# Kernel optimization log

Hardware: AMD Instinct MI355X
Metric: run time of the kernel (lower is better)

## Reference

```python
import jax, jax.numpy as jnp
import numpy as np

D_MODEL = 2048
N_HEADS = 16
D_HEAD = D_MODEL // N_HEADS  # 128
WINDOW = 512
SCALE = D_HEAD ** -0.5


def setup_inputs() -> dict:
    key = jax.random.key(0)
    ks = jax.random.split(key, 5)
    B, S = 2, 4096
    x = jax.random.normal(ks[0], (B, S, D_MODEL), dtype=jnp.float32)
    W_qkv = jax.random.normal(ks[1], (D_MODEL, 3 * D_MODEL), dtype=jnp.float32) * (D_MODEL ** -0.5)
    b_qkv = jax.random.normal(ks[2], (3 * D_MODEL,), dtype=jnp.float32) * 0.02
    W_out = jax.random.normal(ks[3], (D_MODEL, D_MODEL), dtype=jnp.float32) * (D_MODEL ** -0.5)
    b_out = jax.random.normal(ks[4], (D_MODEL,), dtype=jnp.float32) * 0.02
    return {"x": x, "W_qkv": W_qkv, "b_qkv": b_qkv, "W_out": W_out, "b_out": b_out}


def reference(x, W_qkv, b_qkv, W_out, b_out):
    B, S, D = x.shape
    nb = S // WINDOW  # number of independent causal windows (block-diagonal attention)
    qkv = x @ W_qkv + b_qkv  # (B,S,3D)
    q, k, v = jnp.split(qkv, 3, axis=-1)

    def to_blocks(t):
        # (B,S,D) -> (B,H,nb,W,dh)
        return t.reshape(B, nb, WINDOW, N_HEADS, D_HEAD).transpose(0, 3, 1, 2, 4)

    q, k, v = to_blocks(q), to_blocks(k), to_blocks(v)
    # per-window attention scores: (B,H,nb,W,W)
    scores = jnp.einsum('bhnqd,bhnkd->bhnqk', q, k) * SCALE
    causal = jnp.tril(jnp.ones((WINDOW, WINDOW), dtype=bool))
    scores = jnp.where(causal, scores, -jnp.inf)
    attn = jax.nn.softmax(scores, axis=-1)
    out = jnp.einsum('bhnqk,bhnkd->bhnqd', attn, v)  # (B,H,nb,W,dh)
    out = out.transpose(0, 2, 3, 1, 4).reshape(B, S, D)
    return out @ W_out + b_out
```

## Files before the change

kernel.cpp:

```cpp
#include <hip/hip_runtime.h>
#include <stdint.h>


typedef unsigned short u16;
typedef unsigned int u32;
typedef __attribute__((ext_vector_type(8))) short bf16x8;
typedef __attribute__((ext_vector_type(4))) float f32x4;

#define QKN 4096
#define DM 2048

__device__ __forceinline__ u16 f2b(float f) {
  u32 u = __builtin_bit_cast(u32, f);
  u32 r = (u + 0x7fffu + ((u >> 16) & 1u)) >> 16;
  return (u16)r;
}

__device__ __forceinline__ u32 cvt_pk_bf16(float lo, float hi) {
  u32 r;
  asm("v_cvt_pk_bf16_f32 %0, %1, %2" : "=v"(r) : "v"(lo), "v"(hi));
  return r;
}

__device__ __forceinline__ void gload_lds16(const void* g, void* l) {
  __builtin_amdgcn_global_load_lds((const __attribute__((address_space(1))) void*)g,
                                   (__attribute__((address_space(3))) void*)l,
                                   16, 0, 0);
}


__global__ void cast_f32_bf16(const float4* __restrict__ x, uint4* __restrict__ o) {
  int idx = blockIdx.x * 256 + threadIdx.x;
  float4 a = x[2 * idx];
  float4 b = x[2 * idx + 1];
  uint4 r;
  r.x = (u32)f2b(a.x) | ((u32)f2b(a.y) << 16);
  r.y = (u32)f2b(a.z) | ((u32)f2b(a.w) << 16);
  r.z = (u32)f2b(b.x) | ((u32)f2b(b.y) << 16);
  r.w = (u32)f2b(b.z) | ((u32)f2b(b.w) << 16);
  o[idx] = r;
}

__global__ void transpose_cast(const float* __restrict__ W, u16* __restrict__ Wt,
                               int K, int N) {
  __shared__ u16 tile[64][65];
  int tx = threadIdx.x & 63;
  int ty = threadIdx.x >> 6;
  int n0 = blockIdx.x * 64;
  int k0 = blockIdx.y * 64;
#pragma unroll
  for (int r = 0; r < 64; r += 4)
    tile[r + ty][tx] = f2b(W[(size_t)(k0 + r + ty) * N + n0 + tx]);
  __syncthreads();
#pragma unroll
  for (int r = 0; r < 64; r += 4)
    Wt[(size_t)(n0 + r + ty) * K + k0 + tx] = tile[tx][r + ty];
}


template <typename TO>
__global__ __launch_bounds__(256, 3) void gemm_bt(const u16* __restrict__ A,
                                                  const u16* __restrict__ Bt,
                                                  const float* __restrict__ bias,
                                                  TO* __restrict__ C,
                                                  u16* __restrict__ vt,
                                                  int M, int N, int K,
                                                  int crstride, int vstart) {
  __shared__ u16 As[128 * 64];
  __shared__ u16 Bs[128 * 64];
  const int tid = threadIdx.x;
  const int lane = tid & 63;
  const int wave = tid >> 6;
  const int quad = lane >> 4;
  const int l15 = lane & 15;
  const int m0 = blockIdx.y * 128;
  const int n0 = blockIdx.x * 128;
  const int wm = (wave & 1) * 64;
  const int wn = (wave >> 1) * 64;

  f32x4 acc[4][4] = {};

  for (int k0 = 0; k0 < K; k0 += 64) {
#pragma unroll
    for (int i = 0; i < 4; ++i) {
      int sb = wave * 256 + i * 64;
      int s = sb + lane;
      int m = s >> 3;
      int c = (s & 7) ^ (m & 7);
      gload_lds16(A + (size_t)(m0 + m) * K + (k0 + c * 8), As + sb * 8);
      gload_lds16(Bt + (size_t)(n0 + m) * K + (k0 + c * 8), Bs + sb * 8);
    }
    __syncthreads();
#pragma unroll
    for (int ks = 0; ks < 2; ++ks) {
      bf16x8 af[4], bf[4];
#pragma unroll
      for (int i = 0; i < 4; ++i) {
        int m = wm + i * 16 + l15;
        af[i] = *(const bf16x8*)(As + m * 64 + (((ks * 4 + quad) ^ (m & 7)) << 3));
        int n = wn + i * 16 + l15;
        bf[i] = *(const bf16x8*)(Bs + n * 64 + (((ks * 4 + quad) ^ (n & 7)) << 3));
      }
#pragma unroll
      for (int i = 0; i < 4; ++i)
#pragma unroll
        for (int j = 0; j < 4; ++j)
          acc[i][j] = __builtin_amdgcn_mfma_f32_16x16x32_bf16(af[i], bf[j], acc[i][j], 0, 0, 0);
    }
    __syncthreads();
  }

  if (n0 >= vstart) {
#pragma unroll
    for (int j = 0; j < 4; ++j) {
      int col = n0 + wn + j * 16 + l15;
      float bv = bias[col];
      u16* vcol = vt + (size_t)(col - vstart) * 8192;
#pragma unroll
      for (int i = 0; i < 4; ++i) {
        int row = m0 + wm + i * 16 + quad * 4;
        uint2 pk;
        pk.x = (u32)f2b(acc[i][j][0] + bv) | ((u32)f2b(acc[i][j][1] + bv) << 16);
        pk.y = (u32)f2b(acc[i][j][2] + bv) | ((u32)f2b(acc[i][j][3] + bv) << 16);
        *(uint2*)(vcol + row) = pk;
      }
    }
  } else {
#pragma unroll
    for (int j = 0; j < 4; ++j) {
      int col = n0 + wn + j * 16 + l15;
      float bv = bias[col];
#pragma unroll
      for (int i = 0; i < 4; ++i) {
        int row = m0 + wm + i * 16 + quad * 4;
#pragma unroll
        for (int t = 0; t < 4; ++t) {
          float v = acc[i][j][t] + bv;
          if constexpr (sizeof(TO) == 2)
            C[(size_t)(row + t) * crstride + col] = (TO)f2b(v);
          else
            C[(size_t)(row + t) * crstride + col] = (TO)v;
        }
      }
    }
  }
}


__global__ __launch_bounds__(256, 2) void attn_win(const u16* __restrict__ qk,
                                                   const u16* __restrict__ vt,
                                                   u16* __restrict__ attn_out) {
  __shared__ u16 Vs[2][8192];
  __shared__ u16 Ps[128 * 64];
  const int tid = threadIdx.x;
  const int lane = tid & 63;
  const int wave = tid >> 6;
  const int quad = lane >> 4;
  const int l15 = lane & 15;
  const int qt = blockIdx.x;
  const int win = blockIdx.y;
  const int b = blockIdx.z >> 4;
  const int h = blockIdx.z & 15;
  const int tokw = b * 4096 + win * 512;
  const int tokq = tokw + qt * 128;
  const float CL2E = 0.12751743f;
  const float THR = 12.0f;

  auto stageV = [&](int jt, int buf) {
    const u16* vbase = vt + (size_t)(h * 128) * 8192 + (tokw + jt * 64);
    char* dst0 = (char*)Vs[buf] + wave * 1024;
#pragma unroll
    for (int it = 0; it < 4; ++it) {
      int ch = it * 256 + wave * 64 + lane;
      int row = ch >> 3;
      int c = (ch & 7) ^ (row & 7);
      gload_lds16(vbase + (size_t)row * 8192 + c * 8, dst0 + it * 4096);
    }
  };

  stageV(0, 0);

  bf16x8 qf[2][4];
  {
    const u16* Qb = qk + (size_t)tokq * QKN + h * 128;
#pragma unroll
    for (int j = 0; j < 2; ++j) {
      const u16* Qr = Qb + (size_t)(wave * 32 + j * 16 + l15) * QKN + quad * 8;
#pragma unroll
      for (int ks = 0; ks < 4; ++ks)
        qf[j][ks] = *(const bf16x8*)(Qr + ks * 32);
    }
  }

  f32x4 acc_o[8][2] = {};
  float mrun[2] = {-1e30f, -1e30f};
  float lrun[2] = {0.f, 0.f};

  const int jt_end = 2 * qt + 1;
  for (int jt = 0; jt <= jt_end; ++jt) {
    if (jt < jt_end) stageV(jt + 1, (jt + 1) & 1);

    f32x4 acc_s[4][2] = {};
    {
      const u16* Kb = qk + (size_t)(tokw + jt * 64) * QKN + 2048 + h * 128;
      bf16x8 kf[4][4];
#pragma unroll
      for (int i = 0; i < 4; ++i) {
        const u16* Kr = Kb + (size_t)(i * 16 + l15) * QKN + quad * 8;
#pragma unroll
        for (int ks = 0; ks < 4; ++ks)
          kf[i][ks] = *(const bf16x8*)(Kr + ks * 32);
      }
#pragma unroll
      for (int ks = 0; ks < 4; ++ks)
#pragma unroll
        for (int i = 0; i < 4; ++i)
#pragma unroll
          for (int j = 0; j < 2; ++j)
            acc_s[i][j] = __builtin_amdgcn_mfma_f32_16x16x32_bf16(kf[i][ks], qf[j][ks],
                                                                  acc_s[i][j], 0, 0, 0);
    }

    const bool need_mask = (jt >= 2 * qt);
#pragma unroll
    for (int j = 0; j < 2; ++j) {
      int ql = wave * 32 + j * 16 + l15;
      int qg = qt * 128 + ql;
      float vmax = -1e30f;
#pragma unroll
      for (int i = 0; i < 4; ++i)
#pragma unroll
        for (int t = 0; t < 4; ++t) {
          float s = acc_s[i][j][t] * CL2E;
          if (need_mask) {
            int kg = jt * 64 + i * 16 + quad * 4 + t;
            if (kg > qg) s = -1e30f;
          }
          acc_s[i][j][t] = s;
          vmax = fmaxf(vmax, s);
        }
      vmax = fmaxf(vmax, __shfl_xor(vmax, 16));
      vmax = fmaxf(vmax, __shfl_xor(vmax, 32));
      if (__any(vmax > mrun[j] + THR)) {
        float mnew = fmaxf(mrun[j], vmax);
        float alpha = __builtin_amdgcn_exp2f(mrun[j] - mnew);
        mrun[j] = mnew;
        lrun[j] *= alpha;
#pragma unroll
        for (int i2 = 0; i2 < 8; ++i2)
#pragma unroll
          for (int t = 0; t < 4; ++t)
            acc_o[i2][j][t] *= alpha;
      }
      float mnew = mrun[j];
      float vsum = 0.f;
#pragma unroll
      for (int i = 0; i < 4; ++i) {
        float p0 = __builtin_amdgcn_exp2f(acc_s[i][j][0] - mnew);
        float p1 = __builtin_amdgcn_exp2f(acc_s[i][j][1] - mnew);
        float p2 = __builtin_amdgcn_exp2f(acc_s[i][j][2] - mnew);
        float p3 = __builtin_amdgcn_exp2f(acc_s[i][j][3] - mnew);
        vsum += (p0 + p1) + (p2 + p3);
        uint2 pk;
        pk.x = cvt_pk_bf16(p0, p1);
        pk.y = cvt_pk_bf16(p2, p3);
        int kk = i * 16 + quad * 4;
        *(uint2*)((char*)Ps + ql * 128 + (((kk >> 3) ^ (ql & 7)) << 4) + ((kk & 7) << 1)) = pk;
      }
      vsum += __shfl_xor(vsum, 16);
      vsum += __shfl_xor(vsum, 32);
      lrun[j] += vsum;
    }
    __syncthreads();

    const u16* Vtile = Vs[jt & 1];
#pragma unroll
    for (int ks = 0; ks < 2; ++ks) {
      int kk = ks * 32 + quad * 8;
      int kc = kk >> 3;
      bf16x8 pf[2];
#pragma unroll
      for (int j = 0; j < 2; ++j) {
        int ql = wave * 32 + j * 16 + l15;
        pf[j] = *(const bf16x8*)((char*)Ps + ql * 128 + ((kc ^ (ql & 7)) << 4));
      }
#pragma unroll
      for (int i2 = 0; i2 < 8; ++i2) {
        int d = i2 * 16 + l15;
        bf16x8 vf = *(const bf16x8*)((char*)Vtile + d * 128 + ((kc ^ (d & 7)) << 4));
#pragma unroll
        for (int j = 0; j < 2; ++j)
          acc_o[i2][j] = __builtin_amdgcn_mfma_f32_16x16x32_bf16(vf, pf[j], acc_o[i2][j], 0, 0, 0);
      }
    }
    __syncthreads();
  }

#pragma unroll
  for (int j = 0; j < 2; ++j) {
    float inv = 1.0f / lrun[j];
    int ql = wave * 32 + j * 16 + l15;
    u16* orow = attn_out + (size_t)(tokq + ql) * DM + h * 128;
#pragma unroll
    for (int i2 = 0; i2 < 8; ++i2) {
      int d = i2 * 16 + quad * 4;
      uint2 pk;
      pk.x = cvt_pk_bf16(acc_o[i2][j][0] * inv, acc_o[i2][j][1] * inv);
      pk.y = cvt_pk_bf16(acc_o[i2][j][2] * inv, acc_o[i2][j][3] * inv);
      *(uint2*)(orow + d) = pk;
    }
  }
}


extern "C" void kernel_launch(void* const* d_in, const int* in_sizes, int n_in,
                              void* d_out, int out_size, void* d_ws, size_t ws_size,
                              hipStream_t stream) {
  const float* x = (const float*)d_in[0];
  const float* W_qkv = (const float*)d_in[1];
  const float* b_qkv = (const float*)d_in[2];
  const float* W_out = (const float*)d_in[3];
  const float* b_out = (const float*)d_in[4];
  float* out = (float*)d_out;

  char* w = (char*)d_ws;
  u16* xb = (u16*)w;
  u16* wqkvT = (u16*)(w + (32u << 20));
  u16* woutT = (u16*)(w + (56u << 20));
  u16* qk = (u16*)(w + (64u << 20));
  u16* vtb = (u16*)(w + (128u << 20));

  cast_f32_bf16<<<8192, 256, 0, stream>>>((const float4*)x, (uint4*)xb);
  transpose_cast<<<dim3(96, 32), 256, 0, stream>>>(W_qkv, wqkvT, 2048, 6144);
  transpose_cast<<<dim3(32, 32), 256, 0, stream>>>(W_out, woutT, 2048, 2048);
  gemm_bt<u16><<<dim3(48, 64), 256, 0, stream>>>(xb, wqkvT, b_qkv, qk, vtb,
                                                 8192, 6144, 2048, 4096, 4096);
  attn_win<<<dim3(4, 8, 32), 256, 0, stream>>>(qk, vtb, xb);
  gemm_bt<float><<<dim3(16, 64), 256, 0, stream>>>(xb, woutT, b_out, out, vtb,
                                                   8192, 2048, 2048, 2048, 1 << 28);
}
```

Before: 534.3 us.

## Stage K tiles through LDS and pair causal query tiles per block

K tiles are now loaded asynchronously into double-buffered shared memory, using the same swizzled layout as V. Previously every wave read K directly from global memory, and now all four waves share one copy. Each block now processes two query tiles, qt and 3-qt, so every block does the same amount of causal work, and the grid shrinks by half. The extra 32KB of LDS may lower occupancy, and halving the block count reduces parallelism: 512 blocks now, against 1024 before.

```diff
diff --git a/kernel.cpp b/kernel.cpp
--- a/kernel.cpp
+++ b/kernel.cpp
@@ -150,6 +150,7 @@
 __global__ __launch_bounds__(256, 2) void attn_win(const u16* __restrict__ qk,
                                                    const u16* __restrict__ vt,
                                                    u16* __restrict__ attn_out) {
+  __shared__ u16 Ks[2][8192];
   __shared__ u16 Vs[2][8192];
   __shared__ u16 Ps[128 * 64];
   const int tid = threadIdx.x;
@@ -157,12 +158,10 @@
   const int wave = tid >> 6;
   const int quad = lane >> 4;
   const int l15 = lane & 15;
-  const int qt = blockIdx.x;
   const int win = blockIdx.y;
   const int b = blockIdx.z >> 4;
   const int h = blockIdx.z & 15;
   const int tokw = b * 4096 + win * 512;
-  const int tokq = tokw + qt * 128;
   const float CL2E = 0.12751743f;
   const float THR = 12.0f;
 
@@ -177,137 +176,163 @@
       gload_lds16(vbase + (size_t)row * 8192 + c * 8, dst0 + it * 4096);
     }
   };
-
-  stageV(0, 0);
-
-  bf16x8 qf[2][4];
-  {
-    const u16* Qb = qk + (size_t)tokq * QKN + h * 128;
-#pragma unroll
-    for (int j = 0; j < 2; ++j) {
-      const u16* Qr = Qb + (size_t)(wave * 32 + j * 16 + l15) * QKN + quad * 8;
-#pragma unroll
-      for (int ks = 0; ks < 4; ++ks)
-        qf[j][ks] = *(const bf16x8*)(Qr + ks * 32);
-    }
-  }
-
-  f32x4 acc_o[8][2] = {};
-  float mrun[2] = {-1e30f, -1e30f};
-  float lrun[2] = {0.f, 0.f};
-
-  const int jt_end = 2 * qt + 1;
-  for (int jt = 0; jt <= jt_end; ++jt) {
-    if (jt < jt_end) stageV(jt + 1, (jt + 1) & 1);
-
-    f32x4 acc_s[4][2] = {};
+  auto stageK = [&](int jt, int buf) {
+    const u16* kbase = qk + (size_t)(tokw + jt * 64) * QKN + 2048 + h * 128;
+    char* dst0 = (char*)Ks[buf] + wave * 1024;
+#pragma unroll
+    for (int it = 0; it < 4; ++it) {
+      int ch = it * 256 + wave * 64 + lane;
+      int row = ch >> 4;
+      int c16 = ch & 15;
+      int c = (c16 & 8) | ((c16 & 7) ^ (row & 7));
+      gload_lds16(kbase + (size_t)row * QKN + c * 8, dst0 + it * 4096);
+    }
+  };
+
+  const int rx = l15 & 7;
+
+  for (int half = 0; half < 2; ++half) {
+    const int qt = half == 0 ? (int)blockIdx.x : 3 - (int)blockIdx.x;
+    const int tokq = tokw + qt * 128;
+    const int jt_end = 2 * qt + 1;
+
+    stageK(0, 0);
+    stageV(0, 0);
+
+    bf16x8 qf[2][4];
     {
-      const u16* Kb = qk + (size_t)(tokw + jt * 64) * QKN + 2048 + h * 128;
-      bf16x8 kf[4][4];
-#pragma unroll
-      for (int i = 0; i < 4; ++i) {
-        const u16* Kr = Kb + (size_t)(i * 16 + l15) * QKN + quad * 8;
+      const u16* Qb = qk + (size_t)tokq * QKN + h * 128;
+#pragma unroll
+      for (int j = 0; j < 2; ++j) {
+        const u16* Qr = Qb + (size_t)(wave * 32 + j * 16 + l15) * QKN + quad * 8;
 #pragma unroll
         for (int ks = 0; ks < 4; ++ks)
-          kf[i][ks] = *(const bf16x8*)(Kr + ks * 32);
-      }
-#pragma unroll
-      for (int ks = 0; ks < 4; ++ks)
-#pragma unroll
-        for (int i = 0; i < 4; ++i)
-#pragma unroll
-          for (int j = 0; j < 2; ++j)
-            acc_s[i][j] = __builtin_amdgcn_mfma_f32_16x16x32_bf16(kf[i][ks], qf[j][ks],
-                                                                  acc_s[i][j], 0, 0, 0);
-    }
-
-    const bool need_mask = (jt >= 2 * qt);
-#pragma unroll
-    for (int j = 0; j < 2; ++j) {
-      int ql = wave * 32 + j * 16 + l15;
-      int qg = qt * 128 + ql;
-      float vmax = -1e30f;
-#pragma unroll
-      for (int i = 0; i < 4; ++i)
-#pragma unroll
-        for (int t = 0; t < 4; ++t) {
-          float s = acc_s[i][j][t] * CL2E;
-          if (need_mask) {
-            int kg = jt * 64 + i * 16 + quad * 4 + t;
-            if (kg > qg) s = -1e30f;
+          qf[j][ks] = *(const bf16x8*)(Qr + ks * 32);
+      }
+    }
+
+    f32x4 acc_o[8][2] = {};
+    float mrun[2] = {-1e30f, -1e30f};
+    float lrun[2] = {0.f, 0.f};
+
+    __syncthreads();
+
+    for (int jt = 0; jt <= jt_end; ++jt) {
+      if (jt < jt_end) {
+        stageK(jt + 1, (jt + 1) & 1);
+        stageV(jt + 1, (jt + 1) & 1);
+      }
+
+      f32x4 acc_s[4][2] = {};
+      {
+        const u16* Kt = Ks[jt & 1];
+        bf16x8 kf[4][4];
+#pragma unroll
+        for (int i = 0; i < 4; ++i) {
+          const u16* Kr = Kt + (i * 16 + l15) * 128;
+#pragma unroll
+          for (int ks = 0; ks < 4; ++ks) {
+            int c = quad + ks * 4;
+            kf[i][ks] = *(const bf16x8*)(Kr + (((c & 8) | ((c & 7) ^ rx)) << 3));
           }
-          acc_s[i][j][t] = s;
-          vmax = fmaxf(vmax, s);
-        }
-      vmax = fmaxf(vmax, __shfl_xor(vmax, 16));
-      vmax = fmaxf(vmax, __shfl_xor(vmax, 32));
-      if (__any(vmax > mrun[j] + THR)) {
-        float mnew = fmaxf(mrun[j], vmax);
-        float alpha = __builtin_amdgcn_exp2f(mrun[j] - mnew);
-        mrun[j] = mnew;
-        lrun[j] *= alpha;
-#pragma unroll
-        for (int i2 = 0; i2 < 8; ++i2)
-#pragma unroll
-          for (int t = 0; t < 4; ++t)
-            acc_o[i2][j][t] *= alpha;
-      }
-      float mnew = mrun[j];
-      float vsum = 0.f;
-#pragma unroll
-      for (int i = 0; i < 4; ++i) {
-        float p0 = __builtin_amdgcn_exp2f(acc_s[i][j][0] - mnew);
-        float p1 = __builtin_amdgcn_exp2f(acc_s[i][j][1] - mnew);
-        float p2 = __builtin_amdgcn_exp2f(acc_s[i][j][2] - mnew);
-        float p3 = __builtin_amdgcn_exp2f(acc_s[i][j][3] - mnew);
-        vsum += (p0 + p1) + (p2 + p3);
-        uint2 pk;
-        pk.x = cvt_pk_bf16(p0, p1);
-        pk.y = cvt_pk_bf16(p2, p3);
-        int kk = i * 16 + quad * 4;
-        *(uint2*)((char*)Ps + ql * 128 + (((kk >> 3) ^ (ql & 7)) << 4) + ((kk & 7) << 1)) = pk;
-      }
-      vsum += __shfl_xor(vsum, 16);
-      vsum += __shfl_xor(vsum, 32);
-      lrun[j] += vsum;
-    }
-    __syncthreads();
-
-    const u16* Vtile = Vs[jt & 1];
-#pragma unroll
-    for (int ks = 0; ks < 2; ++ks) {
-      int kk = ks * 32 + quad * 8;
-      int kc = kk >> 3;
-      bf16x8 pf[2];
+        }
+#pragma unroll
+        for (int ks = 0; ks < 4; ++ks)
+#pragma unroll
+          for (int i = 0; i < 4; ++i)
+#pragma unroll
+            for (int j = 0; j < 2; ++j)
+              acc_s[i][j] = __builtin_amdgcn_mfma_f32_16x16x32_bf16(kf[i][ks], qf[j][ks],
+                                                                    acc_s[i][j], 0, 0, 0);
+      }
+
+      const bool need_mask = (jt >= 2 * qt);
 #pragma unroll
       for (int j = 0; j < 2; ++j) {
         int ql = wave * 32 + j * 16 + l15;
-        pf[j] = *(const bf16x8*)((char*)Ps + ql * 128 + ((kc ^ (ql & 7)) << 4));
-      }
+        int qg = qt * 128 + ql;
+        float vmax = -1e30f;
+#pragma unroll
+        for (int i = 0; i < 4; ++i)
+#pragma unroll
+          for (int t = 0; t < 4; ++t) {
+            float s = acc_s[i][j][t] * CL2E;
+            if (need_mask) {
+              int kg = jt * 64 + i * 16 + quad * 4 + t;
+              if (kg > qg) s = -1e30f;
+            }
+            acc_s[i][j][t] = s;
+            vmax = fmaxf(vmax, s);
+          }
+        vmax = fmaxf(vmax, __shfl_xor(vmax, 16));
+        vmax = fmaxf(vmax, __shfl_xor(vmax, 32));
+        if (__any(vmax > mrun[j] + THR)) {
+          float mnew = fmaxf(mrun[j], vmax);
+          float alpha = __builtin_amdgcn_exp2f(mrun[j] - mnew);
+          mrun[j] = mnew;
+          lrun[j] *= alpha;
+#pragma unroll
+          for (int i2 = 0; i2 < 8; ++i2)
+#pragma unroll
+            for (int t = 0; t < 4; ++t)
+              acc_o[i2][j][t] *= alpha;
+        }
+        float mnew = mrun[j];
+        float vsum = 0.f;
+#pragma unroll
+        for (int i = 0; i < 4; ++i) {
+          float p0 = __builtin_amdgcn_exp2f(acc_s[i][j][0] - mnew);
+          float p1 = __builtin_amdgcn_exp2f(acc_s[i][j][1] - mnew);
+          float p2 = __builtin_amdgcn_exp2f(acc_s[i][j][2] - mnew);
+          float p3 = __builtin_amdgcn_exp2f(acc_s[i][j][3] - mnew);
+          vsum += (p0 + p1) + (p2 + p3);
+          uint2 pk;
+          pk.x = cvt_pk_bf16(p0, p1);
+          pk.y = cvt_pk_bf16(p2, p3);
+          int kk = i * 16 + quad * 4;
+          *(uint2*)((char*)Ps + ql * 128 + (((kk >> 3) ^ (ql & 7)) << 4) + ((kk & 7) << 1)) = pk;
+        }
+        vsum += __shfl_xor(vsum, 16);
+        vsum += __shfl_xor(vsum, 32);
+        lrun[j] += vsum;
+      }
+      __syncthreads();
+
+      const u16* Vtile = Vs[jt & 1];
+#pragma unroll
+      for (int ks = 0; ks < 2; ++ks) {
+        int kc = (ks * 32 + quad * 8) >> 3;
+        bf16x8 pf[2];
+#pragma unroll
+        for (int j = 0; j < 2; ++j) {
+          int ql = wave * 32 + j * 16 + l15;
+          pf[j] = *(const bf16x8*)((char*)Ps + ql * 128 + ((kc ^ (ql & 7)) << 4));
+        }
+#pragma unroll
+        for (int i2 = 0; i2 < 8; ++i2) {
+          int d = i2 * 16 + l15;
+          bf16x8 vf = *(const bf16x8*)((char*)Vtile + d * 128 + ((kc ^ (d & 7)) << 4));
+#pragma unroll
+          for (int j = 0; j < 2; ++j)
+            acc_o[i2][j] = __builtin_amdgcn_mfma_f32_16x16x32_bf16(vf, pf[j], acc_o[i2][j], 0, 0, 0);
+        }
+      }
+      __syncthreads();
+    }
+
+#pragma unroll
+    for (int j = 0; j < 2; ++j) {
+      float inv = 1.0f / lrun[j];
+      int ql = wave * 32 + j * 16 + l15;
+      u16* orow = attn_out + (size_t)(tokq + ql) * DM + h * 128;
 #pragma unroll
       for (int i2 = 0; i2 < 8; ++i2) {
-        int d = i2 * 16 + l15;
-        bf16x8 vf = *(const bf16x8*)((char*)Vtile + d * 128 + ((kc ^ (d & 7)) << 4));
-#pragma unroll
-        for (int j = 0; j < 2; ++j)
-          acc_o[i2][j] = __builtin_amdgcn_mfma_f32_16x16x32_bf16(vf, pf[j], acc_o[i2][j], 0, 0, 0);
-      }
-    }
-    __syncthreads();
-  }
-
-#pragma unroll
-  for (int j = 0; j < 2; ++j) {
-    float inv = 1.0f / lrun[j];
-    int ql = wave * 32 + j * 16 + l15;
-    u16* orow = attn_out + (size_t)(tokq + ql) * DM + h * 128;
-#pragma unroll
-    for (int i2 = 0; i2 < 8; ++i2) {
-      int d = i2 * 16 + quad * 4;
-      uint2 pk;
-      pk.x = cvt_pk_bf16(acc_o[i2][j][0] * inv, acc_o[i2][j][1] * inv);
-      pk.y = cvt_pk_bf16(acc_o[i2][j][2] * inv, acc_o[i2][j][3] * inv);
-      *(uint2*)(orow + d) = pk;
+        int d = i2 * 16 + quad * 4;
+        uint2 pk;
+        pk.x = cvt_pk_bf16(acc_o[i2][j][0] * inv, acc_o[i2][j][1] * inv);
+        pk.y = cvt_pk_bf16(acc_o[i2][j][2] * inv, acc_o[i2][j][3] * inv);
+        *(uint2*)(orow + d) = pk;
+      }
     }
   }
 }
@@ -335,7 +360,7 @@
   transpose_cast<<<dim3(32, 32), 256, 0, stream>>>(W_out, woutT, 2048, 2048);
   gemm_bt<u16><<<dim3(48, 64), 256, 0, stream>>>(xb, wqkvT, b_qkv, qk, vtb,
                                                  8192, 6144, 2048, 4096, 4096);
-  attn_win<<<dim3(4, 8, 32), 256, 0, stream>>>(qk, vtb, xb);
+  attn_win<<<dim3(2, 8, 32), 256, 0, stream>>>(qk, vtb, xb);
   gemm_bt<float><<<dim3(16, 64), 256, 0, stream>>>(xb, woutT, b_out, out, vtb,
                                                    8192, 2048, 2048, 2048, 1 << 28);
 }
```

After: 485.1 us. 1.1x faster.
